# Performance work log

Measured on AMD Instinct MI355X. Metric: run time of the kernel, lower is better.

The kernel has to match this reference:

```python
import jax, jax.numpy as jnp
import numpy as np


def _rx(state, theta, axis):
    # Apply RX(theta) to qubit at tensor axis `axis`. state: (B, 2,...,2) complex.
    half = theta * 0.5
    c = jnp.cos(half)
    s = jnp.sin(half)
    a0 = jnp.take(state, 0, axis=axis)
    a1 = jnp.take(state, 1, axis=axis)
    return jnp.stack([c * a0 - 1j * s * a1, c * a1 - 1j * s * a0], axis=axis)


def _cnot(state, w):
    # CNOT with control wire w (axis w+1), target wire w+1 (axis w+2).
    c_ax = w + 1
    s0 = jnp.take(state, 0, axis=c_ax)
    # after removing the control axis, the target axis index becomes c_ax
    s1 = jnp.flip(jnp.take(state, 1, axis=c_ax), axis=c_ax)
    return jnp.stack([s0, s1], axis=c_ax)


def _run_circuit(x, params):
    # x: (B, n) encoding angles; params: (depth, n) trainable RX angles.
    B, n = x.shape
    depth = params.shape[0]
    state = jnp.zeros((B,) + (2,) * n, jnp.complex64)
    state = state.at[(slice(None),) + (0,) * n].set(1.0 + 0.0j)
    # angle encoding: RX(x_w) on each wire
    for w in range(n):
        theta = x[:, w].reshape((B,) + (1,) * (n - 1))
        state = _rx(state, theta, w + 1)
    # variational layers: RX(param) per wire, then CNOT chain
    for d in range(depth):
        for w in range(n):
            state = _rx(state, params[d, w], w + 1)
        for w in range(n - 1):
            state = _cnot(state, w)
    probs = state.real ** 2 + state.imag ** 2  # (B, 2,...,2)
    ez = []
    for w in range(n):
        axes = tuple(a for a in range(1, n + 1) if a != w + 1)
        p = probs.sum(axes)  # (B, 2)
        ez.append(p[:, 0] - p[:, 1])  # <Z_w>
    return jnp.stack(ez, axis=1)  # (B, n)


def setup_inputs() -> dict:
    key = jax.random.key(0)
    k0, k1, k2, k3, k4 = jax.random.split(key, 5)
    seq_len, batch, input_dim = 256, 128, 64
    n_qubits, depth, hidden = 10, 2, 256
    inputs = jax.random.normal(k0, (seq_len, batch, input_dim), jnp.float32)
    mask = jax.random.randint(k1, (seq_len, batch), 0, 2).astype(jnp.int32)
    qparams = jax.random.normal(k2, (4, depth, n_qubits), jnp.float32)
    W = jax.random.normal(k3, (4, hidden, n_qubits), jnp.float32) / np.sqrt(n_qubits)
    b = jax.random.normal(k4, (4, hidden), jnp.float32) * 0.01
    return {"inputs": inputs, "mask": mask, "qparams": qparams, "W": W, "b": b}


def reference(inputs, mask, qparams, W, b):
    seq_len, batch, _ = inputs.shape
    n = qparams.shape[-1]
    hidden = W.shape[1]
    maskf = mask.astype(inputs.dtype)

    circuits4 = jax.vmap(_run_circuit, in_axes=(None, 0))  # over the 4 gates

    def step(carry, xm):
        hx, cx = carry
        x_t, m_t = xm
        q_in = jnp.concatenate([x_t, hx], axis=1)[:, :n]  # (B, n)
        z = circuits4(q_in, qparams)                      # (4, B, n)
        pre = jnp.einsum('gbn,ghn->gbh', z, W) + b[:, None, :]
        f = jax.nn.sigmoid(pre[0])
        i = jax.nn.sigmoid(pre[1])
        g = jnp.tanh(pre[2])
        o = jax.nn.sigmoid(pre[3])
        m = m_t[:, None]
        f = f * m + (1.0 - m)
        i = i * m
        g = g * m
        o = o * m + (1.0 - m)
        cx_new = f * cx + i * g
        hx_new = o * jnp.tanh(cx_new)
        return (hx_new, cx_new), hx_new

    h0 = jnp.zeros((batch, hidden), inputs.dtype)
    c0 = jnp.zeros((batch, hidden), inputs.dtype)
    (hx, cx), outputs = jax.lax.scan(jax.checkpoint(step), (h0, c0), (inputs, maskf))
    return outputs, (hx, cx)
```

## Files before the change

### kernel.cpp

```cpp
#include <hip/hip_runtime.h>

#define T_LEN 256
#define BATCH 128
#define NQ 10
#define NG 4
#define HID 256
#define OUT_HX (T_LEN * BATCH * HID)
#define OUT_CX (OUT_HX + BATCH * HID)

__global__ __launch_bounds__(512) void qlstm_kernel(
    const float* __restrict__ inputs,
    const int*  __restrict__ mask,
    const float* __restrict__ qparams,
    const float* __restrict__ W,
    const float* __restrict__ bias,
    float* __restrict__ out)
{
  const int b    = blockIdx.x;
  const int half = blockIdx.y;
  const int tid  = threadIdx.x;
  const int g    = tid & 3;
  const int ch   = tid >> 2;
  const int h    = half * 128 + ch;

  __shared__ __align__(16) float zs[T_LEN][48];
  __shared__ float mk[T_LEN];
  __shared__ float th0_s[NG * NQ], cth_s[NG * NQ], sth_s[NG * NQ];

  if (tid < NG * NQ) {
    int gg = tid / NQ, k = tid - gg * NQ;
    th0_s[tid] = qparams[gg * 2 * NQ + k];
    float t1   = qparams[gg * 2 * NQ + NQ + k];
    sth_s[tid] = __sinf(t1);
    cth_s[tid] = __cosf(t1);
  }
  for (int t = tid; t < T_LEN; t += 512) mk[t] = (float)mask[t * BATCH + b];
  __syncthreads();

  for (int inst = tid; inst < T_LEN * NG; inst += 512) {
    int t = inst >> 2, gg = inst & 3;
    float cphi[NQ], sphi[NQ];
#pragma unroll
    for (int k = 0; k < NQ; ++k) {
      float ang = inputs[(t * BATCH + b) * 64 + k] + th0_s[gg * NQ + k];
      sphi[k] = __sinf(ang);
      cphi[k] = __cosf(ang);
    }
    const float* cth = cth_s + gg * NQ;
    const float* sth = sth_s + gg * NQ;
#pragma unroll
    for (int w = 0; w < NQ; ++w) {
      float vI, vZ, vY, vX; int js;
      if (w == NQ - 1) { vI = 0.f; vZ = cth[NQ-1]; vY = sth[NQ-1]; vX = 0.f; js = NQ - 2; }
      else             { vI = 1.f; vZ = 0.f; vY = 0.f; vX = 0.f; js = w; }
#pragma unroll
      for (int j = js; j >= 0; --j) {
        float nI = cth[j] * (cphi[j+1] * vZ - sphi[j+1] * vY);
        float nZ = cth[j] * vI;
        float nY = sth[j] * vX;
        float nX = -sth[j] * (sphi[j+1] * vZ + cphi[j+1] * vY);
        vI = nI; vZ = nZ; vY = nY; vX = nX;
      }
      zs[t][gg * 12 + w] = vI + cphi[0] * vZ - sphi[0] * vY;
    }
  }
  __syncthreads();

  float Wreg[NQ];
#pragma unroll
  for (int n = 0; n < NQ; ++n) Wreg[n] = W[(g * HID + h) * NQ + n];
  float bg = bias[g * HID + h];

  const float scale_in = (g == 2) ? -2.f : -1.f;
  const float a_c  = (g == 2) ? 2.f : 1.f;
  const float bt_c = (g == 2) ? -1.f : 0.f;
  const float d_c  = (g == 0 || g == 3) ? 1.f : 0.f;

  const int g12 = g * 12;
  float4 za = *(const float4*)&zs[0][g12];
  float4 zb = *(const float4*)&zs[0][g12 + 4];
  float2 zc = *(const float2*)&zs[0][g12 + 8];
  float mcur = mk[0];

  float c = 0.f, hv = 0.f;
  float* outp = out + b * HID + h;

  for (int t = 0; t < T_LEN; ++t) {
    int tn = (t + 1 < T_LEN) ? t + 1 : t;
    float4 na = *(const float4*)&zs[tn][g12];
    float4 nb = *(const float4*)&zs[tn][g12 + 4];
    float2 nc = *(const float2*)&zs[tn][g12 + 8];
    float mnext = mk[tn];

    float acc0 = fmaf(za.x, Wreg[0], bg);
    acc0 = fmaf(za.y, Wreg[1], acc0);
    acc0 = fmaf(za.z, Wreg[2], acc0);
    acc0 = fmaf(za.w, Wreg[3], acc0);
    acc0 = fmaf(zc.x, Wreg[8], acc0);
    float acc1 = zb.x * Wreg[4];
    acc1 = fmaf(zb.y, Wreg[5], acc1);
    acc1 = fmaf(zb.z, Wreg[6], acc1);
    acc1 = fmaf(zb.w, Wreg[7], acc1);
    acc1 = fmaf(zc.y, Wreg[9], acc1);
    float pre = acc0 + acc1;

    float e = __expf(scale_in * pre);
    float u = __builtin_amdgcn_rcpf(1.f + e);
    float val = fmaf(mcur, fmaf(a_c, u, bt_c), d_c * (1.f - mcur));

    float v1 = __shfl_xor(val, 1, 64);
    float v2 = __shfl_xor(val, 2, 64);
    float v3 = __shfl_xor(v1, 2, 64);

    if (g == 0) {
      c = fmaf(val, c, v1 * v2);
      float e2 = __expf(-2.f * c);
      float tc = fmaf(2.f, __builtin_amdgcn_rcpf(1.f + e2), -1.f);
      hv = v3 * tc;
      outp[t * (BATCH * HID)] = hv;
    }
    za = na; zb = nb; zc = nc; mcur = mnext;
  }
  if (g == 0) {
    out[OUT_HX + b * HID + h] = hv;
    out[OUT_CX + b * HID + h] = c;
  }
}

extern "C" void kernel_launch(void* const* d_in, const int* in_sizes, int n_in,
                              void* d_out, int out_size, void* d_ws, size_t ws_size,
                              hipStream_t stream)
{
  int ii = 0, im = 1, iq = 2, iw = 3, ib = 4;
  for (int i = 0; i < n_in; ++i) {
    switch (in_sizes[i]) {
      case 2097152: ii = i; break;
      case 32768:   im = i; break;
      case 80:      iq = i; break;
      case 10240:   iw = i; break;
      case 1024:    ib = i; break;
      default: break;
    }
  }
  const float* inputs  = (const float*)d_in[ii];
  const int*   mask    = (const int*)d_in[im];
  const float* qparams = (const float*)d_in[iq];
  const float* W       = (const float*)d_in[iw];
  const float* bias    = (const float*)d_in[ib];
  float*       out     = (float*)d_out;

  qlstm_kernel<<<dim3(BATCH, 2), dim3(512), 0, stream>>>(
      inputs, mask, qparams, W, bias, out);
}
```

Measured before the change: 120.2 us.

## Split circuit evaluation into separate kernel and compute all four gates per thread

```diff
diff --git a/kernel.cpp b/kernel.cpp
--- a/kernel.cpp
+++ b/kernel.cpp
@@ -3,15 +3,94 @@
 #define T_LEN 256
 #define BATCH 128
 #define NQ 10
-#define NG 4
 #define HID 256
 #define OUT_HX (T_LEN * BATCH * HID)
 #define OUT_CX (OUT_HX + BATCH * HID)
+#define ZSTRIDE 40
 
-__global__ __launch_bounds__(512) void qlstm_kernel(
+__global__ __launch_bounds__(256) void zker(
     const float* __restrict__ inputs,
+    const float* __restrict__ qparams,
+    float* __restrict__ zws)
+{
+  const int b   = blockIdx.x;
+  const int tq  = blockIdx.y;
+  const int tid = threadIdx.x;
+  const int t   = tq * 64 + (tid >> 2);
+  const int g   = tid & 3;
+
+  float th0[NQ], cth[NQ], sth[NQ];
+#pragma unroll
+  for (int k = 0; k < NQ; ++k) {
+    th0[k]   = qparams[g * 2 * NQ + k];
+    float t1 = qparams[g * 2 * NQ + NQ + k];
+    sth[k] = __sinf(t1);
+    cth[k] = __cosf(t1);
+  }
+  float cphi[NQ], sphi[NQ];
+  const float* xp = inputs + (t * BATCH + b) * 64;
+#pragma unroll
+  for (int k = 0; k < NQ; ++k) {
+    float ang = xp[k] + th0[k];
+    sphi[k] = __sinf(ang);
+    cphi[k] = __cosf(ang);
+  }
+  float* zout = zws + (b * T_LEN + t) * ZSTRIDE + g;
+#pragma unroll
+  for (int w = 0; w < NQ; ++w) {
+    float vI, vZ, vY, vX; int js;
+    if (w == NQ - 1) { vI = 0.f; vZ = cth[NQ-1]; vY = sth[NQ-1]; vX = 0.f; js = NQ - 2; }
+    else             { vI = 1.f; vZ = 0.f; vY = 0.f; vX = 0.f; js = w; }
+#pragma unroll
+    for (int j = js; j >= 0; --j) {
+      float nI = cth[j] * (cphi[j+1] * vZ - sphi[j+1] * vY);
+      float nZ = cth[j] * vI;
+      float nY = sth[j] * vX;
+      float nX = -sth[j] * (sphi[j+1] * vZ + cphi[j+1] * vY);
+      vI = nI; vZ = nZ; vY = nY; vX = nX;
+    }
+    zout[w * 4] = vI + cphi[0] * vZ - sphi[0] * vY;
+  }
+}
+
+#define QSTEP(CUR, NXT, TT)                                              \
+  {                                                                      \
+    const int tnext = ((TT) + 1 < T_LEN) ? (TT) + 1 : T_LEN - 1;         \
+    _Pragma("unroll")                                                    \
+    for (int n = 0; n < NQ; ++n)                                         \
+      NXT[n] = *(const float4*)(zpl + tnext * ZSTRIDE + n * 4);          \
+    const float mN = mk[tnext];                                          \
+    float p0 = bg[0], p1 = bg[1], p2 = bg[2], p3 = bg[3];                \
+    _Pragma("unroll")                                                    \
+    for (int n = 0; n < NQ; ++n) {                                       \
+      p0 = fmaf(CUR[n].x, Wr[0][n], p0);                                 \
+      p1 = fmaf(CUR[n].y, Wr[1][n], p1);                                 \
+      p2 = fmaf(CUR[n].z, Wr[2][n], p2);                                 \
+      p3 = fmaf(CUR[n].w, Wr[3][n], p3);                                 \
+    }                                                                    \
+    const float ef = __builtin_amdgcn_exp2f(p0);                         \
+    const float ei = __builtin_amdgcn_exp2f(p1);                         \
+    const float eg = __builtin_amdgcn_exp2f(p2);                         \
+    const float eo = __builtin_amdgcn_exp2f(p3);                         \
+    const float uf = __builtin_amdgcn_rcpf(1.f + ef);                    \
+    const float ui = __builtin_amdgcn_rcpf(1.f + ei);                    \
+    const float ug = __builtin_amdgcn_rcpf(1.f + eg);                    \
+    const float uo = __builtin_amdgcn_rcpf(1.f + eo);                    \
+    const float onem = 1.f - mcur;                                       \
+    const float fm = fmaf(mcur, uf, onem);                               \
+    const float gb = fmaf(2.f, ug, -1.f);                                \
+    c = fmaf(fm, c, mcur * ui * gb);                                     \
+    const float om = fmaf(mcur, uo, onem);                               \
+    const float ec = __builtin_amdgcn_exp2f(c * KT2);                    \
+    const float tcv = __builtin_amdgcn_rcpf(1.f + ec);                   \
+    hv = om * fmaf(2.f, tcv, -1.f);                                      \
+    out[(TT) * (BATCH * HID) + oidx] = hv;                               \
+    mcur = mN;                                                           \
+  }
+
+__global__ __launch_bounds__(128) void scanker(
+    const float* __restrict__ zws,
     const int*  __restrict__ mask,
-    const float* __restrict__ qparams,
     const float* __restrict__ W,
     const float* __restrict__ bias,
     float* __restrict__ out)
@@ -19,112 +98,42 @@
   const int b    = blockIdx.x;
   const int half = blockIdx.y;
   const int tid  = threadIdx.x;
-  const int g    = tid & 3;
-  const int ch   = tid >> 2;
-  const int h    = half * 128 + ch;
+  const int h    = half * 128 + tid;
 
-  __shared__ __align__(16) float zs[T_LEN][48];
   __shared__ float mk[T_LEN];
-  __shared__ float th0_s[NG * NQ], cth_s[NG * NQ], sth_s[NG * NQ];
-
-  if (tid < NG * NQ) {
-    int gg = tid / NQ, k = tid - gg * NQ;
-    th0_s[tid] = qparams[gg * 2 * NQ + k];
-    float t1   = qparams[gg * 2 * NQ + NQ + k];
-    sth_s[tid] = __sinf(t1);
-    cth_s[tid] = __cosf(t1);
-  }
-  for (int t = tid; t < T_LEN; t += 512) mk[t] = (float)mask[t * BATCH + b];
+  for (int t = tid; t < T_LEN; t += 128) mk[t] = (float)mask[t * BATCH + b];
   __syncthreads();
 
-  for (int inst = tid; inst < T_LEN * NG; inst += 512) {
-    int t = inst >> 2, gg = inst & 3;
-    float cphi[NQ], sphi[NQ];
+  const float KS  = -1.44269504089f;
+  const float KT2 = 2.f * KS;
+
+  float Wr[4][NQ]; float bg[4];
 #pragma unroll
-    for (int k = 0; k < NQ; ++k) {
-      float ang = inputs[(t * BATCH + b) * 64 + k] + th0_s[gg * NQ + k];
-      sphi[k] = __sinf(ang);
-      cphi[k] = __cosf(ang);
-    }
-    const float* cth = cth_s + gg * NQ;
-    const float* sth = sth_s + gg * NQ;
+  for (int g = 0; g < 4; ++g) {
+    const float s = (g == 2) ? KT2 : KS;
 #pragma unroll
-    for (int w = 0; w < NQ; ++w) {
-      float vI, vZ, vY, vX; int js;
-      if (w == NQ - 1) { vI = 0.f; vZ = cth[NQ-1]; vY = sth[NQ-1]; vX = 0.f; js = NQ - 2; }
-      else             { vI = 1.f; vZ = 0.f; vY = 0.f; vX = 0.f; js = w; }
+    for (int n = 0; n < NQ; ++n) Wr[g][n] = W[(g * HID + h) * NQ + n] * s;
+    bg[g] = bias[g * HID + h] * s;
+  }
+
+  int vz; asm volatile("v_mov_b32 %0, 0" : "=v"(vz));
+  const float* zpl = zws + b * T_LEN * ZSTRIDE + vz;
+
+  float4 zA[NQ], zB[NQ];
 #pragma unroll
-      for (int j = js; j >= 0; --j) {
-        float nI = cth[j] * (cphi[j+1] * vZ - sphi[j+1] * vY);
-        float nZ = cth[j] * vI;
-        float nY = sth[j] * vX;
-        float nX = -sth[j] * (sphi[j+1] * vZ + cphi[j+1] * vY);
-        vI = nI; vZ = nZ; vY = nY; vX = nX;
-      }
-      zs[t][gg * 12 + w] = vI + cphi[0] * vZ - sphi[0] * vY;
-    }
-  }
-  __syncthreads();
-
-  float Wreg[NQ];
-#pragma unroll
-  for (int n = 0; n < NQ; ++n) Wreg[n] = W[(g * HID + h) * NQ + n];
-  float bg = bias[g * HID + h];
-
-  const float scale_in = (g == 2) ? -2.f : -1.f;
-  const float a_c  = (g == 2) ? 2.f : 1.f;
-  const float bt_c = (g == 2) ? -1.f : 0.f;
-  const float d_c  = (g == 0 || g == 3) ? 1.f : 0.f;
-
-  const int g12 = g * 12;
-  float4 za = *(const float4*)&zs[0][g12];
-  float4 zb = *(const float4*)&zs[0][g12 + 4];
-  float2 zc = *(const float2*)&zs[0][g12 + 8];
+  for (int n = 0; n < NQ; ++n) zA[n] = *(const float4*)(zpl + n * 4);
   float mcur = mk[0];
 
   float c = 0.f, hv = 0.f;
-  float* outp = out + b * HID + h;
+  const int oidx = b * HID + h;
 
-  for (int t = 0; t < T_LEN; ++t) {
-    int tn = (t + 1 < T_LEN) ? t + 1 : t;
-    float4 na = *(const float4*)&zs[tn][g12];
-    float4 nb = *(const float4*)&zs[tn][g12 + 4];
-    float2 nc = *(const float2*)&zs[tn][g12 + 8];
-    float mnext = mk[tn];
+  for (int t = 0; t < T_LEN; t += 2) {
+    QSTEP(zA, zB, t);
+    QSTEP(zB, zA, t + 1);
+  }
 
-    float acc0 = fmaf(za.x, Wreg[0], bg);
-    acc0 = fmaf(za.y, Wreg[1], acc0);
-    acc0 = fmaf(za.z, Wreg[2], acc0);
-    acc0 = fmaf(za.w, Wreg[3], acc0);
-    acc0 = fmaf(zc.x, Wreg[8], acc0);
-    float acc1 = zb.x * Wreg[4];
-    acc1 = fmaf(zb.y, Wreg[5], acc1);
-    acc1 = fmaf(zb.z, Wreg[6], acc1);
-    acc1 = fmaf(zb.w, Wreg[7], acc1);
-    acc1 = fmaf(zc.y, Wreg[9], acc1);
-    float pre = acc0 + acc1;
-
-    float e = __expf(scale_in * pre);
-    float u = __builtin_amdgcn_rcpf(1.f + e);
-    float val = fmaf(mcur, fmaf(a_c, u, bt_c), d_c * (1.f - mcur));
-
-    float v1 = __shfl_xor(val, 1, 64);
-    float v2 = __shfl_xor(val, 2, 64);
-    float v3 = __shfl_xor(v1, 2, 64);
-
-    if (g == 0) {
-      c = fmaf(val, c, v1 * v2);
-      float e2 = __expf(-2.f * c);
-      float tc = fmaf(2.f, __builtin_amdgcn_rcpf(1.f + e2), -1.f);
-      hv = v3 * tc;
-      outp[t * (BATCH * HID)] = hv;
-    }
-    za = na; zb = nb; zc = nc; mcur = mnext;
-  }
-  if (g == 0) {
-    out[OUT_HX + b * HID + h] = hv;
-    out[OUT_CX + b * HID + h] = c;
-  }
+  out[OUT_HX + oidx] = hv;
+  out[OUT_CX + oidx] = c;
 }
 
 extern "C" void kernel_launch(void* const* d_in, const int* in_sizes, int n_in,
@@ -148,7 +157,8 @@
   const float* W       = (const float*)d_in[iw];
   const float* bias    = (const float*)d_in[ib];
   float*       out     = (float*)d_out;
+  float*       zws     = (float*)d_ws;
 
-  qlstm_kernel<<<dim3(BATCH, 2), dim3(512), 0, stream>>>(
-      inputs, mask, qparams, W, bias, out);
+  zker<<<dim3(BATCH, 4), dim3(256), 0, stream>>>(inputs, qparams, zws);
+  scanker<<<dim3(BATCH, 2), dim3(128), 0, stream>>>(zws, mask, W, bias, out);
 }
```

Result: slower. 169.3 us (+40.9%).
